# Performance work log

Measured on AMD Instinct MI355X. Metric: run time of the kernel, lower is better.

## Reference

```python
import jax, jax.numpy as jnp
import numpy as np

B, T, C = 8, 1024, 384
L, H, D, F = 8, 16, 24, 1536
EPS = 1e-5

def _ln(x, g, b):
    m = jnp.mean(x, axis=-1, keepdims=True)
    v = jnp.mean(jnp.square(x - m), axis=-1, keepdims=True)
    return (x - m) * jax.lax.rsqrt(v + EPS) * g + b

def setup_inputs() -> dict:
    key = jax.random.key(0)
    ks = jax.random.split(key, 8)
    s = 0.02
    return {
        "idx": jax.random.uniform(ks[0], (B, T, C), jnp.float32),
        "pos_emb": jax.random.normal(ks[1], (T, C), jnp.float32) * s,
        "Wq": jax.random.normal(ks[2], (L, H, C, D), jnp.float32) * s,
        "Wk": jax.random.normal(ks[3], (L, H, C, D), jnp.float32) * s,
        "Wv": jax.random.normal(ks[4], (L, H, C, D), jnp.float32) * s,
        "Wo": jax.random.normal(ks[5], (L, C, C), jnp.float32) * s,
        "bo": jnp.zeros((L, C), jnp.float32),
        "ln1_g": jnp.ones((L, C), jnp.float32),
        "ln1_b": jnp.zeros((L, C), jnp.float32),
        "ln2_g": jnp.ones((L, C), jnp.float32),
        "ln2_b": jnp.zeros((L, C), jnp.float32),
        "W1": jax.random.normal(ks[6], (L, C, F), jnp.float32) * s,
        "b1": jnp.zeros((L, F), jnp.float32),
        "W2": jax.random.normal(ks[7], (L, F, C), jnp.float32) * s,
        "b2": jnp.zeros((L, C), jnp.float32),
        "lnf_g": jnp.ones((C,), jnp.float32),
        "lnf_b": jnp.zeros((C,), jnp.float32),
    }

def reference(idx, pos_emb, Wq, Wk, Wv, Wo, bo, ln1_g, ln1_b, ln2_g, ln2_b,
              W1, b1, W2, b2, lnf_g, lnf_b):
    Bc, Tc, Cc = idx.shape
    x = idx + pos_emb[:Tc]
    causal = jnp.tril(jnp.ones((Tc, Tc), bool))  # [T,T]
    scale = D ** -0.5
    for l in range(L):
        h = _ln(x, ln1_g[l], ln1_b[l])
        q = jnp.einsum('btc,hcd->bhtd', h, Wq[l])
        k = jnp.einsum('btc,hcd->bhtd', h, Wk[l])
        v = jnp.einsum('btc,hcd->bhtd', h, Wv[l])
        wei = jnp.einsum('bhtd,bhsd->bhts', q, k) * scale
        wei = jnp.where(causal, wei, -jnp.inf)
        wei = jax.nn.softmax(wei, axis=-1)
        o = jnp.einsum('bhts,bhsd->bhtd', wei, v)
        o = o.transpose(0, 2, 1, 3).reshape(Bc, Tc, H * D)
        x = x + o @ Wo[l] + bo[l]
        h2 = _ln(x, ln2_g[l], ln2_b[l])
        x = x + jax.nn.relu(h2 @ W1[l] + b1[l]) @ W2[l] + b2[l]
    x = _ln(x, lnf_g, lnf_b)
    return jax.nn.relu(x)  # MSE path with targets=None
```

## Files before the change

### kernel.cpp

```cpp
#include <hip/hip_runtime.h>

#define B_ 8
#define T_ 1024
#define C_ 384
#define L_ 8
#define H_ 16
#define D_ 24
#define F_ 1536
#define M_ 8192

using bf16x8 = __attribute__((ext_vector_type(8))) __bf16;
using f32x4  = __attribute__((ext_vector_type(4))) float;

__device__ __forceinline__ ushort f2b(float f) {
  union { float f; unsigned u; } cv; cv.f = f;
  unsigned u = cv.u;
  return (ushort)((u + 0x7FFFu + ((u >> 16) & 1u)) >> 16);
}

__global__ __launch_bounds__(256) void k_embed(const float* __restrict__ idx,
                                               const float* __restrict__ pos,
                                               float* __restrict__ x) {
  long i4 = ((long)blockIdx.x * 256 + threadIdx.x) * 4;
  float4 a = *(const float4*)(idx + i4);
  long p = i4 % (long)(T_ * C_);
  float4 b = *(const float4*)(pos + p);
  a.x += b.x; a.y += b.y; a.z += b.z; a.w += b.w;
  *(float4*)(x + i4) = a;
}

__global__ __launch_bounds__(256) void k_ln(const float* __restrict__ x,
                                            const float* __restrict__ g,
                                            const float* __restrict__ b,
                                            ushort* __restrict__ out) {
  int row  = blockIdx.x * 4 + (threadIdx.x >> 6);
  int lane = threadIdx.x & 63;
  const float* xr = x + (long)row * C_;
  float v[6]; float sum = 0.f;
#pragma unroll
  for (int i = 0; i < 3; ++i) {
    float2 t = *(const float2*)(xr + 2*(lane + 64*i));
    v[2*i] = t.x; v[2*i+1] = t.y; sum += t.x + t.y;
  }
#pragma unroll
  for (int m = 1; m < 64; m <<= 1) sum += __shfl_xor(sum, m);
  float mean = sum * (1.f / C_);
  float vs = 0.f;
#pragma unroll
  for (int i = 0; i < 6; ++i) { float d = v[i] - mean; vs += d * d; }
#pragma unroll
  for (int m = 1; m < 64; m <<= 1) vs += __shfl_xor(vs, m);
  float rstd = rsqrtf(vs * (1.f / C_) + 1e-5f);
  ushort* orow = out + (long)row * C_;
#pragma unroll
  for (int i = 0; i < 3; ++i) {
    int c = 2*(lane + 64*i);
    float2 gg = *(const float2*)(g + c);
    float2 bb = *(const float2*)(b + c);
    ushort2 w;
    w.x = f2b((v[2*i]   - mean) * rstd * gg.x + bb.x);
    w.y = f2b((v[2*i+1] - mean) * rstd * gg.y + bb.y);
    *(ushort2*)(orow + c) = w;
  }
}

__global__ __launch_bounds__(256) void k_lnf(const float* __restrict__ x,
                                             const float* __restrict__ g,
                                             const float* __restrict__ b,
                                             float* __restrict__ out) {
  int row  = blockIdx.x * 4 + (threadIdx.x >> 6);
  int lane = threadIdx.x & 63;
  const float* xr = x + (long)row * C_;
  float v[6]; float sum = 0.f;
#pragma unroll
  for (int i = 0; i < 3; ++i) {
    float2 t = *(const float2*)(xr + 2*(lane + 64*i));
    v[2*i] = t.x; v[2*i+1] = t.y; sum += t.x + t.y;
  }
#pragma unroll
  for (int m = 1; m < 64; m <<= 1) sum += __shfl_xor(sum, m);
  float mean = sum * (1.f / C_);
  float vs = 0.f;
#pragma unroll
  for (int i = 0; i < 6; ++i) { float d = v[i] - mean; vs += d * d; }
#pragma unroll
  for (int m = 1; m < 64; m <<= 1) vs += __shfl_xor(vs, m);
  float rstd = rsqrtf(vs * (1.f / C_) + 1e-5f);
  float* orow = out + (long)row * C_;
#pragma unroll
  for (int i = 0; i < 3; ++i) {
    int c = 2*(lane + 64*i);
    float2 gg = *(const float2*)(g + c);
    float2 bb = *(const float2*)(b + c);
    float2 w;
    w.x = fmaxf((v[2*i]   - mean) * rstd * gg.x + bb.x, 0.f);
    w.y = fmaxf((v[2*i+1] - mean) * rstd * gg.y + bb.y, 0.f);
    *(float2*)(orow + c) = w;
  }
}

__global__ __launch_bounds__(256) void k_trans_qkv(const float* __restrict__ src,
                                                   ushort* __restrict__ dst, int which) {
  __shared__ float tile[32][33];
  int z = blockIdx.z;
  int l = z >> 4, hh = z & 15;
  const float* sb = src + (long)z * C_ * D_;
  ushort* db = dst + (long)l * (3*C_) * C_ + (long)(which * C_ + hh * D_) * C_;
  int r0 = blockIdx.y * 32;
  int tx = threadIdx.x & 31, ty = threadIdx.x >> 5;
#pragma unroll
  for (int i = 0; i < 32; i += 8)
    tile[ty + i][tx] = (tx < D_) ? sb[(long)(r0 + ty + i) * D_ + tx] : 0.f;
  __syncthreads();
#pragma unroll
  for (int i = 0; i < 32; i += 8) {
    int s = ty + i, r = r0 + tx;
    if (s < D_) db[(long)s * C_ + r] = f2b(tile[tx][ty + i]);
  }
}

__global__ __launch_bounds__(256) void k_trans_w(const float* __restrict__ src,
                                                 ushort* __restrict__ dst, int R, int S) {
  __shared__ float tile[32][33];
  const float* sb = src + (long)blockIdx.z * R * S;
  ushort* db = dst + (long)blockIdx.z * R * S;
  int r0 = blockIdx.y * 32, s0 = blockIdx.x * 32;
  int tx = threadIdx.x & 31, ty = threadIdx.x >> 5;
#pragma unroll
  for (int i = 0; i < 32; i += 8) {
    int r = r0 + ty + i, s = s0 + tx;
    tile[ty + i][tx] = (r < R && s < S) ? sb[(long)r * S + s] : 0.f;
  }
  __syncthreads();
#pragma unroll
  for (int i = 0; i < 32; i += 8) {
    int s = s0 + ty + i, r = r0 + tx;
    if (s < S && r < R) db[(long)s * R + r] = f2b(tile[tx][ty + i]);
  }
}

__global__ __launch_bounds__(256) void k_gemm(const ushort* __restrict__ A, int lda,
                                              const ushort* __restrict__ Bt, int ldb,
                                              const float* __restrict__ bias,
                                              const float* resid,
                                              float* outF,
                                              ushort* outB,
                                              int N, int K, int relu) {
  __shared__ ushort As[128 * 64];
  __shared__ ushort Bs[128 * 64];
  int m0 = blockIdx.y * 128, n0 = blockIdx.x * 128;
  int tid = threadIdx.x, lane = tid & 63, wid = tid >> 6;
  int wr = (wid >> 1) * 64, wc = (wid & 1) * 64;
  int g = lane >> 4, q = lane & 15;
  f32x4 acc[4][4] = {};

  for (int k0 = 0; k0 < K; k0 += 64) {
    __syncthreads();
#pragma unroll
    for (int it = 0; it < 4; ++it) {
      int idx = tid + it * 256;
      int r = idx >> 3, c8 = (idx & 7) << 3;
      int sw = ((r * 64 + c8) * 2) ^ ((r & 7) << 4);
      uint4 av = *(const uint4*)(A + (long)(m0 + r) * lda + k0 + c8);
      *(uint4*)((char*)As + sw) = av;
      uint4 bv = *(const uint4*)(Bt + (long)(n0 + r) * ldb + k0 + c8);
      *(uint4*)((char*)Bs + sw) = bv;
    }
    __syncthreads();
#pragma unroll
    for (int kk = 0; kk < 2; ++kk) {
      bf16x8 af[4], bfr[4];
#pragma unroll
      for (int mi = 0; mi < 4; ++mi) {
        int row = wr + mi * 16 + q;
        int byt = ((row * 64 + kk * 32 + g * 8) * 2) ^ ((row & 7) << 4);
        af[mi] = *(const bf16x8*)((const char*)As + byt);
      }
#pragma unroll
      for (int ni = 0; ni < 4; ++ni) {
        int row = wc + ni * 16 + q;
        int byt = ((row * 64 + kk * 32 + g * 8) * 2) ^ ((row & 7) << 4);
        bfr[ni] = *(const bf16x8*)((const char*)Bs + byt);
      }
#pragma unroll
      for (int mi = 0; mi < 4; ++mi)
#pragma unroll
        for (int ni = 0; ni < 4; ++ni)
          acc[mi][ni] = __builtin_amdgcn_mfma_f32_16x16x32_bf16(af[mi], bfr[ni], acc[mi][ni], 0, 0, 0);
    }
  }
#pragma unroll
  for (int mi = 0; mi < 4; ++mi)
#pragma unroll
    for (int ni = 0; ni < 4; ++ni) {
      int rb = m0 + wr + mi * 16 + g * 4;
      int cc = n0 + wc + ni * 16 + q;
      float bv = bias ? bias[cc] : 0.f;
#pragma unroll
      for (int j = 0; j < 4; ++j) {
        long off = (long)(rb + j) * N + cc;
        float val = acc[mi][ni][j] + bv;
        if (resid) val += resid[off];
        if (relu)  val = fmaxf(val, 0.f);
        if (outF)  outF[off] = val;
        if (outB)  outB[off] = f2b(val);
      }
    }
}

__global__ __launch_bounds__(256) void k_attn(const ushort* __restrict__ qkv,
                                              ushort* __restrict__ o) {
  __shared__ ushort Qs[64 * 40];
  __shared__ ushort Ks[128 * 40];
  __shared__ ushort Vts[32 * 136];
  __shared__ ushort Ps[64 * 136];

  int t0 = blockIdx.x * 64;
  int bh = blockIdx.y; int b = bh >> 4, hh = bh & 15;
  int tid = threadIdx.x, lane = tid & 63, w = tid >> 6;
  int g = lane >> 4, q = lane & 15;
  long baseQ = (long)b * T_ * 1152 + hh * D_;
  long baseK = baseQ + 384;
  long baseV = baseQ + 768;
  const float scale = 0.20412414523193154f;
  const f32x4 zf = {0.f, 0.f, 0.f, 0.f};

  for (int i = tid; i < 8 * 136; i += 256) Vts[24 * 136 + i] = 0;
  {
    int r = tid >> 2, c8 = (tid & 3) << 3;
    uint4 val = {0, 0, 0, 0};
    if (c8 < D_) val = *(const uint4*)(qkv + baseQ + (long)(t0 + r) * 1152 + c8);
    *(uint4*)(&Qs[r * 40 + c8]) = val;
  }
  __syncthreads();
  bf16x8 qa = *(const bf16x8*)(&Qs[(w * 16 + q) * 40 + g * 8]);

  f32x4 acc0 = zf, acc1 = zf;
  float lsum[4] = {0.f, 0.f, 0.f, 0.f};

  int send = t0 + 64;
  for (int s0 = 0; s0 < send; s0 += 128) {
    __syncthreads();
#pragma unroll
    for (int it = 0; it < 2; ++it) {
      int idx = tid + it * 256;
      int r = idx >> 2, c8 = (idx & 3) << 3;
      uint4 val = {0, 0, 0, 0};
      if (c8 < D_) val = *(const uint4*)(qkv + baseK + (long)(s0 + r) * 1152 + c8);
      *(uint4*)(&Ks[r * 40 + c8]) = val;
      if (c8 < D_) {
        uint4 vv = *(const uint4*)(qkv + baseV + (long)(s0 + r) * 1152 + c8);
        const ushort* pv = (const ushort*)&vv;
#pragma unroll
        for (int e = 0; e < 8; ++e) Vts[(c8 + e) * 136 + r] = pv[e];
      }
    }
    __syncthreads();
#pragma unroll
    for (int si = 0; si < 8; ++si) {
      bf16x8 kb = *(const bf16x8*)(&Ks[(si * 16 + q) * 40 + g * 8]);
      f32x4 sc = __builtin_amdgcn_mfma_f32_16x16x32_bf16(qa, kb, zf, 0, 0, 0);
      int s_abs = s0 + si * 16 + q;
#pragma unroll
      for (int j = 0; j < 4; ++j) {
        int t_abs = t0 + w * 16 + g * 4 + j;
        float p = (s_abs <= t_abs) ? __expf(sc[j] * scale) : 0.f;
        lsum[j] += p;
        Ps[(w * 16 + g * 4 + j) * 136 + si * 16 + q] = f2b(p);
      }
    }
    __syncthreads();
#pragma unroll
    for (int kk = 0; kk < 4; ++kk) {
      bf16x8 pa  = *(const bf16x8*)(&Ps[(w * 16 + q) * 136 + kk * 32 + g * 8]);
      bf16x8 vb0 = *(const bf16x8*)(&Vts[q * 136 + kk * 32 + g * 8]);
      acc0 = __builtin_amdgcn_mfma_f32_16x16x32_bf16(pa, vb0, acc0, 0, 0, 0);
      bf16x8 vb1 = *(const bf16x8*)(&Vts[(16 + q) * 136 + kk * 32 + g * 8]);
      acc1 = __builtin_amdgcn_mfma_f32_16x16x32_bf16(pa, vb1, acc1, 0, 0, 0);
    }
  }
#pragma unroll
  for (int m = 1; m < 16; m <<= 1)
#pragma unroll
    for (int j = 0; j < 4; ++j) lsum[j] += __shfl_xor(lsum[j], m);
#pragma unroll
  for (int j = 0; j < 4; ++j) {
    float inv = 1.f / lsum[j];
    int t_abs = t0 + w * 16 + g * 4 + j;
    long orow = (long)(b * T_ + t_abs) * C_ + hh * D_;
    o[orow + q] = f2b(acc0[j] * inv);
    if (q < 8) o[orow + 16 + q] = f2b(acc1[j] * inv);
  }
}

extern "C" void kernel_launch(void* const* d_in, const int* in_sizes, int n_in,
                              void* d_out, int out_size, void* d_ws, size_t ws_size,
                              hipStream_t stream) {
  (void)in_sizes; (void)n_in; (void)out_size; (void)ws_size;
  const float* idx  = (const float*)d_in[0];
  const float* pos  = (const float*)d_in[1];
  const float* Wq   = (const float*)d_in[2];
  const float* Wk   = (const float*)d_in[3];
  const float* Wv   = (const float*)d_in[4];
  const float* Wo   = (const float*)d_in[5];
  const float* bo   = (const float*)d_in[6];
  const float* ln1g = (const float*)d_in[7];
  const float* ln1b = (const float*)d_in[8];
  const float* ln2g = (const float*)d_in[9];
  const float* ln2b = (const float*)d_in[10];
  const float* W1   = (const float*)d_in[11];
  const float* b1   = (const float*)d_in[12];
  const float* W2   = (const float*)d_in[13];
  const float* b2   = (const float*)d_in[14];
  const float* lnfg = (const float*)d_in[15];
  const float* lnfb = (const float*)d_in[16];

  char* ws = (char*)d_ws;
  float*  x     = (float*)(ws);
  ushort* h     = (ushort*)(ws + 12582912);
  ushort* qkv   = (ushort*)(ws + 18874368);
  ushort* o     = (ushort*)(ws + 37748736);
  ushort* u     = (ushort*)(ws + 44040192);
  ushort* WqkvT = (ushort*)(ws + 69206016);
  ushort* WoT   = (ushort*)(ws + 76283904);
  ushort* W1T   = (ushort*)(ws + 78643200);
  ushort* W2T   = (ushort*)(ws + 88080384);

  k_trans_qkv<<<dim3(1, 12, L_ * H_), 256, 0, stream>>>(Wq, WqkvT, 0);
  k_trans_qkv<<<dim3(1, 12, L_ * H_), 256, 0, stream>>>(Wk, WqkvT, 1);
  k_trans_qkv<<<dim3(1, 12, L_ * H_), 256, 0, stream>>>(Wv, WqkvT, 2);
  k_trans_w<<<dim3(12, 12, L_), 256, 0, stream>>>(Wo, WoT, C_, C_);
  k_trans_w<<<dim3(48, 12, L_), 256, 0, stream>>>(W1, W1T, C_, F_);
  k_trans_w<<<dim3(12, 48, L_), 256, 0, stream>>>(W2, W2T, F_, C_);

  k_embed<<<(M_ * C_) / (256 * 4), 256, 0, stream>>>(idx, pos, x);

  for (int l = 0; l < L_; ++l) {
    k_ln<<<M_ / 4, 256, 0, stream>>>(x, ln1g + l * C_, ln1b + l * C_, h);
    k_gemm<<<dim3(1152 / 128, M_ / 128), 256, 0, stream>>>(
        h, C_, WqkvT + (long)l * 1152 * C_, C_,
        nullptr, nullptr, nullptr, qkv, 1152, C_, 0);
    k_attn<<<dim3(T_ / 64, B_ * H_), 256, 0, stream>>>(qkv, o);
    k_gemm<<<dim3(C_ / 128, M_ / 128), 256, 0, stream>>>(
        o, C_, WoT + (long)l * C_ * C_, C_,
        bo + l * C_, x, x, nullptr, C_, C_, 0);
    k_ln<<<M_ / 4, 256, 0, stream>>>(x, ln2g + l * C_, ln2b + l * C_, h);
    k_gemm<<<dim3(F_ / 128, M_ / 128), 256, 0, stream>>>(
        h, C_, W1T + (long)l * F_ * C_, C_,
        b1 + l * F_, nullptr, nullptr, u, F_, C_, 1);
    k_gemm<<<dim3(C_ / 128, M_ / 128), 256, 0, stream>>>(
        u, F_, W2T + (long)l * C_ * F_, F_,
        b2 + l * C_, x, x, nullptr, C_, F_, 0);
  }
  k_lnf<<<M_ / 4, 256, 0, stream>>>(x, lnfg, lnfb, (float*)d_out);
}
```

Before: 1.756 ms.

## Use direct-to-LDS loads in GEMM, emit transposed V, and drop attention LDS staging

The GEMM now loads A and B tiles with global_load_lds, using a swizzled source address, instead of going through registers. It is also templated on a BN tile width so the N=384 GEMMs run with 64-wide tiles and get more blocks. The QKV GEMM epilogue writes V directly in a transposed per-head layout, which is zeroed once with memset. This lets attention read Q, K and Vt straight from global memory without LDS staging or block-wide syncs, and skip fully masked sub-tiles. The risk is uncoalesced global reads in attention and a changed workspace layout.

```diff
diff --git a/kernel.cpp b/kernel.cpp
--- a/kernel.cpp
+++ b/kernel.cpp
@@ -16,6 +16,14 @@
   union { float f; unsigned u; } cv; cv.f = f;
   unsigned u = cv.u;
   return (ushort)((u + 0x7FFFu + ((u >> 16) & 1u)) >> 16);
+}
+__device__ __forceinline__ ushort f2b_cvt(float f) {
+  __bf16 h = (__bf16)f;
+  return *(ushort*)&h;
+}
+__device__ __forceinline__ void gload_lds16(const void* g, void* l) {
+  __builtin_amdgcn_global_load_lds((const __attribute__((address_space(1))) void*)g,
+                                   (__attribute__((address_space(3))) void*)l, 16, 0, 0);
 }
 
 __global__ __launch_bounds__(256) void k_embed(const float* __restrict__ idx,
@@ -139,39 +147,48 @@
   }
 }
 
+template<int BN>
 __global__ __launch_bounds__(256) void k_gemm(const ushort* __restrict__ A, int lda,
                                               const ushort* __restrict__ Bt, int ldb,
                                               const float* __restrict__ bias,
                                               const float* resid,
-                                              float* outF,
-                                              ushort* outB,
+                                              float* outF, ushort* outB, ushort* vtOut,
                                               int N, int K, int relu) {
   __shared__ ushort As[128 * 64];
-  __shared__ ushort Bs[128 * 64];
-  int m0 = blockIdx.y * 128, n0 = blockIdx.x * 128;
+  __shared__ ushort Bs[BN * 64];
+  constexpr int ITB = BN / 32;
+  constexpr int MF  = (BN == 128) ? 4 : 2;
+  int m0 = blockIdx.y * 128, n0 = blockIdx.x * BN;
   int tid = threadIdx.x, lane = tid & 63, wid = tid >> 6;
-  int wr = (wid >> 1) * 64, wc = (wid & 1) * 64;
+  int wr = (BN == 128) ? (wid >> 1) * 64 : wid * 32;
+  int wc = (BN == 128) ? (wid & 1) * 64 : 0;
   int g = lane >> 4, q = lane & 15;
-  f32x4 acc[4][4] = {};
+  f32x4 acc[MF][4] = {};
 
   for (int k0 = 0; k0 < K; k0 += 64) {
     __syncthreads();
 #pragma unroll
     for (int it = 0; it < 4; ++it) {
       int idx = tid + it * 256;
-      int r = idx >> 3, c8 = (idx & 7) << 3;
-      int sw = ((r * 64 + c8) * 2) ^ ((r & 7) << 4);
-      uint4 av = *(const uint4*)(A + (long)(m0 + r) * lda + k0 + c8);
-      *(uint4*)((char*)As + sw) = av;
-      uint4 bv = *(const uint4*)(Bt + (long)(n0 + r) * ldb + k0 + c8);
-      *(uint4*)((char*)Bs + sw) = bv;
+      int r = idx >> 3;
+      int ch = ((idx & 7) ^ (r & 7)) << 3;
+      gload_lds16(A + (long)(m0 + r) * lda + k0 + ch,
+                  (char*)As + (wid * 64 + it * 256) * 16);
+    }
+#pragma unroll
+    for (int it = 0; it < ITB; ++it) {
+      int idx = tid + it * 256;
+      int r = idx >> 3;
+      int ch = ((idx & 7) ^ (r & 7)) << 3;
+      gload_lds16(Bt + (long)(n0 + r) * ldb + k0 + ch,
+                  (char*)Bs + (wid * 64 + it * 256) * 16);
     }
     __syncthreads();
 #pragma unroll
     for (int kk = 0; kk < 2; ++kk) {
-      bf16x8 af[4], bfr[4];
-#pragma unroll
-      for (int mi = 0; mi < 4; ++mi) {
+      bf16x8 af[MF], bfr[4];
+#pragma unroll
+      for (int mi = 0; mi < MF; ++mi) {
         int row = wr + mi * 16 + q;
         int byt = ((row * 64 + kk * 32 + g * 8) * 2) ^ ((row & 7) << 4);
         af[mi] = *(const bf16x8*)((const char*)As + byt);
@@ -183,100 +200,100 @@
         bfr[ni] = *(const bf16x8*)((const char*)Bs + byt);
       }
 #pragma unroll
-      for (int mi = 0; mi < 4; ++mi)
+      for (int mi = 0; mi < MF; ++mi)
 #pragma unroll
         for (int ni = 0; ni < 4; ++ni)
           acc[mi][ni] = __builtin_amdgcn_mfma_f32_16x16x32_bf16(af[mi], bfr[ni], acc[mi][ni], 0, 0, 0);
     }
   }
 #pragma unroll
-  for (int mi = 0; mi < 4; ++mi)
+  for (int mi = 0; mi < MF; ++mi)
 #pragma unroll
     for (int ni = 0; ni < 4; ++ni) {
       int rb = m0 + wr + mi * 16 + g * 4;
       int cc = n0 + wc + ni * 16 + q;
       float bv = bias ? bias[cc] : 0.f;
+      float vals[4];
 #pragma unroll
       for (int j = 0; j < 4; ++j) {
-        long off = (long)(rb + j) * N + cc;
         float val = acc[mi][ni][j] + bv;
-        if (resid) val += resid[off];
+        if (resid) val += resid[(long)(rb + j) * N + cc];
         if (relu)  val = fmaxf(val, 0.f);
-        if (outF)  outF[off] = val;
-        if (outB)  outB[off] = f2b(val);
+        vals[j] = val;
+      }
+      if (vtOut && cc >= 768) {
+        int dcol = cc - 768;
+        int hh2 = (dcol * 43691) >> 20;
+        int dd = dcol - hh2 * 24;
+        int bb = rb >> 10, tt = rb & 1023;
+        ushort4 w4 = { f2b(vals[0]), f2b(vals[1]), f2b(vals[2]), f2b(vals[3]) };
+        *(ushort4*)(vtOut + ((long)((bb * 16 + hh2) * 32 + dd) << 10) + tt) = w4;
+      } else {
+#pragma unroll
+        for (int j = 0; j < 4; ++j) {
+          long off = (long)(rb + j) * N + cc;
+          if (outF) outF[off] = vals[j];
+          if (outB) outB[off] = f2b(vals[j]);
+        }
       }
     }
 }
 
 __global__ __launch_bounds__(256) void k_attn(const ushort* __restrict__ qkv,
+                                              const ushort* __restrict__ Vt,
                                               ushort* __restrict__ o) {
-  __shared__ ushort Qs[64 * 40];
-  __shared__ ushort Ks[128 * 40];
-  __shared__ ushort Vts[32 * 136];
-  __shared__ ushort Ps[64 * 136];
-
+  __shared__ ushort Ps[4][16][136];
   int t0 = blockIdx.x * 64;
-  int bh = blockIdx.y; int b = bh >> 4, hh = bh & 15;
+  int bh = blockIdx.y, b = bh >> 4, hh = bh & 15;
   int tid = threadIdx.x, lane = tid & 63, w = tid >> 6;
   int g = lane >> 4, q = lane & 15;
-  long baseQ = (long)b * T_ * 1152 + hh * D_;
-  long baseK = baseQ + 384;
-  long baseV = baseQ + 768;
   const float scale = 0.20412414523193154f;
   const f32x4 zf = {0.f, 0.f, 0.f, 0.f};
 
-  for (int i = tid; i < 8 * 136; i += 256) Vts[24 * 136 + i] = 0;
-  {
-    int r = tid >> 2, c8 = (tid & 3) << 3;
-    uint4 val = {0, 0, 0, 0};
-    if (c8 < D_) val = *(const uint4*)(qkv + baseQ + (long)(t0 + r) * 1152 + c8);
-    *(uint4*)(&Qs[r * 40 + c8]) = val;
-  }
-  __syncthreads();
-  bf16x8 qa = *(const bf16x8*)(&Qs[(w * 16 + q) * 40 + g * 8]);
+  bf16x8 qa = {};
+  if (g < 3) qa = *(const bf16x8*)(qkv + (long)(b * T_ + t0 + w * 16 + q) * 1152 + hh * D_ + g * 8);
+  const ushort* kbase = qkv + (long)b * T_ * 1152 + 384 + hh * D_;
+  const ushort* vtb   = Vt + (long)bh * 32 * 1024;
 
   f32x4 acc0 = zf, acc1 = zf;
   float lsum[4] = {0.f, 0.f, 0.f, 0.f};
-
   int send = t0 + 64;
+
   for (int s0 = 0; s0 < send; s0 += 128) {
-    __syncthreads();
-#pragma unroll
-    for (int it = 0; it < 2; ++it) {
-      int idx = tid + it * 256;
-      int r = idx >> 2, c8 = (idx & 3) << 3;
-      uint4 val = {0, 0, 0, 0};
-      if (c8 < D_) val = *(const uint4*)(qkv + baseK + (long)(s0 + r) * 1152 + c8);
-      *(uint4*)(&Ks[r * 40 + c8]) = val;
-      if (c8 < D_) {
-        uint4 vv = *(const uint4*)(qkv + baseV + (long)(s0 + r) * 1152 + c8);
-        const ushort* pv = (const ushort*)&vv;
-#pragma unroll
-        for (int e = 0; e < 8; ++e) Vts[(c8 + e) * 136 + r] = pv[e];
-      }
-    }
-    __syncthreads();
+    int rem = send - s0;
+    int siMax = (rem >= 128) ? 8 : (rem >> 4);
+    int kkMax = (rem >= 128) ? 4 : (rem >> 5);
+    f32x4 sc[8];
 #pragma unroll
     for (int si = 0; si < 8; ++si) {
-      bf16x8 kb = *(const bf16x8*)(&Ks[(si * 16 + q) * 40 + g * 8]);
-      f32x4 sc = __builtin_amdgcn_mfma_f32_16x16x32_bf16(qa, kb, zf, 0, 0, 0);
-      int s_abs = s0 + si * 16 + q;
-#pragma unroll
-      for (int j = 0; j < 4; ++j) {
-        int t_abs = t0 + w * 16 + g * 4 + j;
-        float p = (s_abs <= t_abs) ? __expf(sc[j] * scale) : 0.f;
-        lsum[j] += p;
-        Ps[(w * 16 + g * 4 + j) * 136 + si * 16 + q] = f2b(p);
-      }
-    }
-    __syncthreads();
+      if (si < siMax) {
+        bf16x8 kb = {};
+        if (g < 3) kb = *(const bf16x8*)(kbase + (long)(s0 + si * 16 + q) * 1152 + g * 8);
+        sc[si] = __builtin_amdgcn_mfma_f32_16x16x32_bf16(qa, kb, zf, 0, 0, 0);
+      }
+    }
+#pragma unroll
+    for (int si = 0; si < 8; ++si) {
+      if (si < siMax) {
+        int s_abs = s0 + si * 16 + q;
+#pragma unroll
+        for (int j = 0; j < 4; ++j) {
+          int t_abs = t0 + w * 16 + g * 4 + j;
+          float p = (s_abs <= t_abs) ? __expf(sc[si][j] * scale) : 0.f;
+          lsum[j] += p;
+          Ps[w][g * 4 + j][si * 16 + q] = f2b_cvt(p);
+        }
+      }
+    }
 #pragma unroll
     for (int kk = 0; kk < 4; ++kk) {
-      bf16x8 pa  = *(const bf16x8*)(&Ps[(w * 16 + q) * 136 + kk * 32 + g * 8]);
-      bf16x8 vb0 = *(const bf16x8*)(&Vts[q * 136 + kk * 32 + g * 8]);
-      acc0 = __builtin_amdgcn_mfma_f32_16x16x32_bf16(pa, vb0, acc0, 0, 0, 0);
-      bf16x8 vb1 = *(const bf16x8*)(&Vts[(16 + q) * 136 + kk * 32 + g * 8]);
-      acc1 = __builtin_amdgcn_mfma_f32_16x16x32_bf16(pa, vb1, acc1, 0, 0, 0);
+      if (kk < kkMax) {
+        bf16x8 pa  = *(const bf16x8*)(&Ps[w][q][kk * 32 + g * 8]);
+        bf16x8 vb0 = *(const bf16x8*)(vtb + (long)q * 1024 + s0 + kk * 32 + g * 8);
+        acc0 = __builtin_amdgcn_mfma_f32_16x16x32_bf16(pa, vb0, acc0, 0, 0, 0);
+        bf16x8 vb1 = *(const bf16x8*)(vtb + (long)(16 + q) * 1024 + s0 + kk * 32 + g * 8);
+        acc1 = __builtin_amdgcn_mfma_f32_16x16x32_bf16(pa, vb1, acc1, 0, 0, 0);
+      }
     }
   }
 #pragma unroll
@@ -319,12 +336,14 @@
   float*  x     = (float*)(ws);
   ushort* h     = (ushort*)(ws + 12582912);
   ushort* qkv   = (ushort*)(ws + 18874368);
-  ushort* o     = (ushort*)(ws + 37748736);
-  ushort* u     = (ushort*)(ws + 44040192);
-  ushort* WqkvT = (ushort*)(ws + 69206016);
-  ushort* WoT   = (ushort*)(ws + 76283904);
-  ushort* W1T   = (ushort*)(ws + 78643200);
-  ushort* W2T   = (ushort*)(ws + 88080384);
+  ushort* u     = (ushort*)(ws + 37748736);
+  ushort* Vt    = (ushort*)(ws + 62914560);
+  ushort* WqkvT = (ushort*)(ws + 71303168);
+  ushort* WoT   = (ushort*)(ws + 78381056);
+  ushort* W1T   = (ushort*)(ws + 80740352);
+  ushort* W2T   = (ushort*)(ws + 90177536);
+
+  hipMemsetAsync(Vt, 0, 8388608, stream);
 
   k_trans_qkv<<<dim3(1, 12, L_ * H_), 256, 0, stream>>>(Wq, WqkvT, 0);
   k_trans_qkv<<<dim3(1, 12, L_ * H_), 256, 0, stream>>>(Wk, WqkvT, 1);
@@ -337,20 +356,20 @@
 
   for (int l = 0; l < L_; ++l) {
     k_ln<<<M_ / 4, 256, 0, stream>>>(x, ln1g + l * C_, ln1b + l * C_, h);
-    k_gemm<<<dim3(1152 / 128, M_ / 128), 256, 0, stream>>>(
+    k_gemm<128><<<dim3(1152 / 128, M_ / 128), 256, 0, stream>>>(
         h, C_, WqkvT + (long)l * 1152 * C_, C_,
-        nullptr, nullptr, nullptr, qkv, 1152, C_, 0);
-    k_attn<<<dim3(T_ / 64, B_ * H_), 256, 0, stream>>>(qkv, o);
-    k_gemm<<<dim3(C_ / 128, M_ / 128), 256, 0, stream>>>(
-        o, C_, WoT + (long)l * C_ * C_, C_,
-        bo + l * C_, x, x, nullptr, C_, C_, 0);
+        nullptr, nullptr, nullptr, qkv, Vt, 1152, C_, 0);
+    k_attn<<<dim3(T_ / 64, B_ * H_), 256, 0, stream>>>(qkv, Vt, h);
+    k_gemm<64><<<dim3(C_ / 64, M_ / 128), 256, 0, stream>>>(
+        h, C_, WoT + (long)l * C_ * C_, C_,
+        bo + l * C_, x, x, nullptr, nullptr, C_, C_, 0);
     k_ln<<<M_ / 4, 256, 0, stream>>>(x, ln2g + l * C_, ln2b + l * C_, h);
-    k_gemm<<<dim3(F_ / 128, M_ / 128), 256, 0, stream>>>(
+    k_gemm<128><<<dim3(F_ / 128, M_ / 128), 256, 0, stream>>>(
         h, C_, W1T + (long)l * F_ * C_, C_,
-        b1 + l * F_, nullptr, nullptr, u, F_, C_, 1);
-    k_gemm<<<dim3(C_ / 128, M_ / 128), 256, 0, stream>>>(
+        b1 + l * F_, nullptr, nullptr, u, nullptr, F_, C_, 1);
+    k_gemm<64><<<dim3(C_ / 64, M_ / 128), 256, 0, stream>>>(
         u, F_, W2T + (long)l * C_ * F_, F_,
-        b2 + l * C_, x, x, nullptr, C_, F_, 0);
+        b2 + l * C_, x, x, nullptr, nullptr, C_, F_, 0);
   }
   k_lnf<<<M_ / 4, 256, 0, stream>>>(x, lnfg, lnfb, (float*)d_out);
 }
```

After: 2.067 ms. 17.7% more time.
